# Performance work log

Measured on AMD Instinct MI355X. Metric: run time of the kernel, lower is better.

Reference implementation:

```python
import jax, jax.numpy as jnp
import numpy as np

C_M, C_Z, H, C = 256, 128, 8, 32  # msa emb, pair emb, heads, head channels
S, R = 128, 256                   # MSA rows, residues


def layer_norm(x, gamma, beta, eps=1e-5):
    mu = jnp.mean(x, axis=-1, keepdims=True)
    var = jnp.var(x, axis=-1, keepdims=True)
    return (x - mu) * jax.lax.rsqrt(var + eps) * gamma + beta


def setup_inputs() -> dict:
    key = jax.random.key(0)
    ks = jax.random.split(key, 12)
    sc_m = 1.0 / np.sqrt(C_M)
    sc_z = 1.0 / np.sqrt(C_Z)
    sc_hc = 1.0 / np.sqrt(H * C)
    return {
        "msa_rep": jax.random.normal(ks[0], (S, R, C_M), dtype=jnp.float32),
        "pair_rep": jax.random.normal(ks[1], (R, R, C_Z), dtype=jnp.float32),
        "ln_msa_g": jnp.ones((C_M,), jnp.float32),
        "ln_msa_b": jnp.zeros((C_M,), jnp.float32),
        "ln_pair_g": jnp.ones((C_Z,), jnp.float32),
        "ln_pair_b": jnp.zeros((C_Z,), jnp.float32),
        "w_q": jax.random.normal(ks[2], (C_M, H, C), jnp.float32) * sc_m,
        "w_k": jax.random.normal(ks[3], (C_M, H, C), jnp.float32) * sc_m,
        "w_v": jax.random.normal(ks[4], (C_M, H, C), jnp.float32) * sc_m,
        "w_g": jax.random.normal(ks[5], (C_M, H, C), jnp.float32) * sc_m,
        "b_g": jnp.zeros((H, C), jnp.float32),
        "w_b": jax.random.normal(ks[6], (C_Z, H), jnp.float32) * sc_z,
        "b_b": jnp.zeros((H,), jnp.float32),
        "w_o": jax.random.normal(ks[7], (H, C, C_M), jnp.float32) * sc_hc,
        "b_o": jnp.zeros((C_M,), jnp.float32),
    }


def reference(msa_rep, pair_rep, ln_msa_g, ln_msa_b, ln_pair_g, ln_pair_b,
              w_q, w_k, w_v, w_g, b_g, w_b, b_b, w_o, b_o):
    m = layer_norm(msa_rep, ln_msa_g, ln_msa_b)                 # [S,R,C_M]
    q = jnp.einsum('src,chd->srhd', m, w_q)                     # [S,R,H,C]
    k = jnp.einsum('src,chd->srhd', m, w_k)
    v = jnp.einsum('src,chd->srhd', m, w_v)
    gates = jax.nn.sigmoid(jnp.einsum('src,chd->srhd', m, w_g) + b_g)
    # pair bias: [R,R,H] -> [H,R,R]
    z = layer_norm(pair_rep, ln_pair_g, ln_pair_b)
    b = jnp.einsum('ijc,ch->hij', z, w_b) + b_b[:, None, None]  # [H,R,R]
    logits = jnp.einsum('sqhd,skhd->shqk', q, k) / np.sqrt(C)   # [S,H,R,R]
    logits = logits + b[None]
    w = jax.nn.softmax(logits, axis=-1)
    o = jnp.einsum('shqk,skhd->sqhd', w, v)                     # [S,R,H,C]
    o = gates * o
    out = jnp.einsum('srhd,hdc->src', o, w_o) + b_o             # [S,R,C_M]
    return out
```

## Files before the change

### kernel.cpp

```cpp
#include <hip/hip_runtime.h>
#include <hip/hip_bf16.h>

#define S_DIM 128
#define R_DIM 256
#define CM 256
#define CZ 128
#define H_DIM 8
#define C_DIM 32

typedef short bf16x8 __attribute__((ext_vector_type(8)));
typedef float f32x4 __attribute__((ext_vector_type(4)));

__device__ inline ushort f2b(float f) {
  __hip_bfloat16 b = __float2bfloat16(f);
  return *(ushort*)&b;
}
__device__ inline float b2f(ushort u) {
  __hip_bfloat16 b = *(__hip_bfloat16*)&u;
  return __bfloat162float(b);
}

__device__ __forceinline__ void gld_lds16(const ushort* g, ushort* l) {
  __builtin_amdgcn_global_load_lds(
      (const __attribute__((address_space(1))) unsigned int*)g,
      (__attribute__((address_space(3))) unsigned int*)l, 16, 0, 0);
}

__global__ __launch_bounds__(256) void wt_kernel(
    const float* __restrict__ wq, const float* __restrict__ wk,
    const float* __restrict__ wv, const float* __restrict__ wg,
    const float* __restrict__ wo, ushort* __restrict__ Wt5) {
  __shared__ float t[64][65];
  int z = blockIdx.z;
  const float* W = (z == 0) ? wq : (z == 1) ? wk : (z == 2) ? wv
                   : (z == 3) ? wg : wo;
  ushort* Wt = Wt5 + (size_t)z * 65536;
  int tid = threadIdx.x;
  int r = tid >> 2, c4 = (tid & 3) * 16;
  int rowBase = blockIdx.y * 64, colBase = blockIdx.x * 64;
#pragma unroll
  for (int j = 0; j < 16; ++j)
    t[r][c4 + j] = W[(size_t)(rowBase + r) * 256 + colBase + c4 + j];
  __syncthreads();
#pragma unroll
  for (int j = 0; j < 16; ++j)
    Wt[(size_t)(colBase + r) * 256 + rowBase + c4 + j] = f2b(t[c4 + j][r]);
}

__global__ __launch_bounds__(256) void ln_msa_kernel(
    const float* __restrict__ x, const float* __restrict__ g,
    const float* __restrict__ b, ushort* __restrict__ m) {
  int lane = threadIdx.x & 63, w = threadIdx.x >> 6;
  int row = blockIdx.x * 4 + w;
  const float* xp = x + (size_t)row * CM + lane * 4;
  float4 v = *(const float4*)xp;
  float s1 = v.x + v.y + v.z + v.w;
  float s2 = v.x * v.x + v.y * v.y + v.z * v.z + v.w * v.w;
#pragma unroll
  for (int off = 32; off; off >>= 1) {
    s1 += __shfl_xor(s1, off, 64);
    s2 += __shfl_xor(s2, off, 64);
  }
  float mean = s1 * (1.0f / CM);
  float rstd = rsqrtf(s2 * (1.0f / CM) - mean * mean + 1e-5f);
  float4 gv = *(const float4*)(g + lane * 4);
  float4 bv = *(const float4*)(b + lane * 4);
  ushort4 o;
  o.x = f2b((v.x - mean) * rstd * gv.x + bv.x);
  o.y = f2b((v.y - mean) * rstd * gv.y + bv.y);
  o.z = f2b((v.z - mean) * rstd * gv.z + bv.z);
  o.w = f2b((v.w - mean) * rstd * gv.w + bv.w);
  *(ushort4*)(m + (size_t)row * CM + lane * 4) = o;
}

__global__ __launch_bounds__(256) void pair_bias_kernel(
    const float* __restrict__ z, const float* __restrict__ g,
    const float* __restrict__ b, const float* __restrict__ w_b,
    const float* __restrict__ b_b, float* __restrict__ bias) {
  __shared__ float wbs[CZ][8];
  __shared__ float gs[CZ], bs[CZ];
  int tid = threadIdx.x;
  if (tid < CZ) { gs[tid] = g[tid]; bs[tid] = b[tid]; }
  for (int i = tid; i < CZ * 8; i += 256) wbs[i >> 3][i & 7] = w_b[i];
  __syncthreads();
  int q = tid & 3;
  int row = blockIdx.x * 64 + (tid >> 2);
  const float* zp = z + (size_t)row * CZ + q * 32;
  float4 v[8];
#pragma unroll
  for (int j = 0; j < 8; ++j) v[j] = *(const float4*)(zp + j * 4);
  float s1 = 0.f, s2 = 0.f;
#pragma unroll
  for (int j = 0; j < 8; ++j) {
    s1 += v[j].x + v[j].y + v[j].z + v[j].w;
    s2 += v[j].x * v[j].x + v[j].y * v[j].y + v[j].z * v[j].z +
          v[j].w * v[j].w;
  }
  s1 += __shfl_xor(s1, 1, 64);
  s2 += __shfl_xor(s2, 1, 64);
  s1 += __shfl_xor(s1, 2, 64);
  s2 += __shfl_xor(s2, 2, 64);
  float mean = s1 * (1.0f / CZ);
  float var = s2 * (1.0f / CZ) - mean * mean;
  float rstd = rsqrtf(var + 1e-5f);
  float acc[8] = {};
#pragma unroll
  for (int j = 0; j < 8; ++j) {
    float e[4] = {v[j].x, v[j].y, v[j].z, v[j].w};
#pragma unroll
    for (int u = 0; u < 4; ++u) {
      int c = q * 32 + j * 4 + u;
      float zn = (e[u] - mean) * rstd * gs[c] + bs[c];
#pragma unroll
      for (int h = 0; h < 8; ++h) acc[h] += zn * wbs[c][h];
    }
  }
#pragma unroll
  for (int h = 0; h < 8; ++h) {
    acc[h] += __shfl_xor(acc[h], 1, 64);
    acc[h] += __shfl_xor(acc[h], 2, 64);
  }
  int h0 = q * 2;
  bias[(size_t)h0 * (R_DIM * R_DIM) + row] = acc[h0] + b_b[h0];
  bias[(size_t)(h0 + 1) * (R_DIM * R_DIM) + row] = acc[h0 + 1] + b_b[h0 + 1];
}

__global__ __launch_bounds__(256) void proj_mfma(
    const ushort* __restrict__ M, const ushort* __restrict__ Wt5,
    const float* __restrict__ b_g, ushort* __restrict__ qb,
    ushort* __restrict__ kb2, ushort* __restrict__ vb,
    ushort* __restrict__ gb) {
  __shared__ ushort As[128 * 64];
  __shared__ ushort Bs[64 * 64];
  int tid = threadIdx.x, lane = tid & 63, wid = tid >> 6;
  int lr = lane & 15, lg = lane >> 4;
  int rowBase = blockIdx.x * 128;
  int cby = blockIdx.y;
  int proj = cby >> 2;
  int sc = (lane & 7) ^ ((lane >> 3) & 7);
  const ushort* Ag =
      M + (size_t)(rowBase + wid * 32 + (lane >> 3)) * 256 + sc * 8;
  const ushort* Bg =
      Wt5 + (size_t)(cby * 64 + wid * 16 + (lane >> 3)) * 256 + sc * 8;
  ushort* Asl = As + wid * (32 * 64);
  ushort* Bsl = Bs + wid * (16 * 64);
  int wr = wid >> 1, wc = wid & 1;
  int sx = (lr & 7) * 8;
  f32x4 zf = {0.f, 0.f, 0.f, 0.f};
  f32x4 acc[4][2];
#pragma unroll
  for (int i = 0; i < 4; ++i)
#pragma unroll
    for (int j = 0; j < 2; ++j) acc[i][j] = zf;

  for (int kb = 0; kb < 4; ++kb) {
    if (kb) __syncthreads();
#pragma unroll
    for (int c = 0; c < 4; ++c)
      gld_lds16(Ag + kb * 64 + c * (8 * 256), Asl + c * (8 * 64));
#pragma unroll
    for (int c = 0; c < 2; ++c)
      gld_lds16(Bg + kb * 64 + c * (8 * 256), Bsl + c * (8 * 64));
    __syncthreads();
#pragma unroll
    for (int kk = 0; kk < 2; ++kk) {
      bf16x8 a[4], b[2];
#pragma unroll
      for (int mf = 0; mf < 4; ++mf)
        a[mf] = *(const bf16x8*)&As[(wr * 64 + mf * 16 + lr) * 64 +
                                    ((kk * 32 + lg * 8) ^ sx)];
#pragma unroll
      for (int nf = 0; nf < 2; ++nf)
        b[nf] = *(const bf16x8*)&Bs[(wc * 32 + nf * 16 + lr) * 64 +
                                    ((kk * 32 + lg * 8) ^ sx)];
#pragma unroll
      for (int mf = 0; mf < 4; ++mf)
#pragma unroll
        for (int nf = 0; nf < 2; ++nf)
          acc[mf][nf] = __builtin_amdgcn_mfma_f32_16x16x32_bf16(
              b[nf], a[mf], acc[mf][nf], 0, 0, 0);
    }
  }
#pragma unroll
  for (int mf = 0; mf < 4; ++mf) {
    int row = rowBase + wr * 64 + mf * 16 + lr;
    int s = row >> 8, rr = row & 255;
#pragma unroll
    for (int nf = 0; nf < 2; ++nf) {
      int colL = (cby & 3) * 64 + wc * 32 + nf * 16 + lg * 4;
      int h = colL >> 5, d0 = colL & 31;
      size_t oidx = ((size_t)((s * H_DIM + h) * R_DIM + rr)) * C_DIM + d0;
      f32x4 v4 = acc[mf][nf];
      ushort4 o4;
      if (proj == 0) {
        o4.x = f2b(v4[0] * 0.17677669529663687f);
        o4.y = f2b(v4[1] * 0.17677669529663687f);
        o4.z = f2b(v4[2] * 0.17677669529663687f);
        o4.w = f2b(v4[3] * 0.17677669529663687f);
        *(ushort4*)(qb + oidx) = o4;
      } else if (proj == 1) {
        o4.x = f2b(v4[0]); o4.y = f2b(v4[1]);
        o4.z = f2b(v4[2]); o4.w = f2b(v4[3]);
        *(ushort4*)(kb2 + oidx) = o4;
      } else if (proj == 2) {
        o4.x = f2b(v4[0]); o4.y = f2b(v4[1]);
        o4.z = f2b(v4[2]); o4.w = f2b(v4[3]);
        *(ushort4*)(vb + oidx) = o4;
      } else {
        float4 bg4 = *(const float4*)(b_g + colL);
        o4.x = f2b(1.f / (1.f + __expf(-(v4[0] + bg4.x))));
        o4.y = f2b(1.f / (1.f + __expf(-(v4[1] + bg4.y))));
        o4.z = f2b(1.f / (1.f + __expf(-(v4[2] + bg4.z))));
        o4.w = f2b(1.f / (1.f + __expf(-(v4[3] + bg4.w))));
        *(ushort4*)(gb + oidx) = o4;
      }
    }
  }
}

__global__ __launch_bounds__(512, 4) void attn_mfma(
    const ushort* __restrict__ q, const ushort* __restrict__ k,
    const ushort* __restrict__ v, const ushort* __restrict__ g,
    const float* __restrict__ bias, ushort* __restrict__ ob) {
  __shared__ ushort Vt[32][264];
  __shared__ ushort Pl[8][32][72];
  int blk = blockIdx.x;
  int s = blk >> 3, h = blk & 7;
  int tid = threadIdx.x, lane = tid & 63, w = tid >> 6;
  int lr = lane & 15, lg = lane >> 4;
  size_t base = (size_t)(s * H_DIM + h) * (R_DIM * C_DIM);

  {
    int key = tid >> 1, half = (tid & 1) * 16;
    const ushort* vp = v + base + (size_t)key * 32 + half;
    bf16x8 t0 = *(const bf16x8*)vp;
    bf16x8 t1 = *(const bf16x8*)(vp + 8);
#pragma unroll
    for (int j = 0; j < 8; ++j) {
      Vt[half + j][key] = (ushort)t0[j];
      Vt[half + 8 + j][key] = (ushort)t1[j];
    }
  }
  __syncthreads();

  int qrow0 = w * 32;
  bf16x8 qf[2];
#pragma unroll
  for (int mf = 0; mf < 2; ++mf)
    qf[mf] = *(const bf16x8*)(q + base + (size_t)(qrow0 + mf * 16 + lr) * 32 +
                              lg * 8);
  const float* bp0 = bias + ((size_t)h * R_DIM + qrow0 + lg * 4) * R_DIM +
                     lr * 4;

  float lsum[2][4] = {};
  f32x4 of[2][2];
  f32x4 zf = {0.f, 0.f, 0.f, 0.f};
#pragma unroll
  for (int mf = 0; mf < 2; ++mf) {
    of[mf][0] = zf;
    of[mf][1] = zf;
  }

  bf16x8 kf[4];
#pragma unroll
  for (int nf = 0; nf < 4; ++nf)
    kf[nf] = *(const bf16x8*)(k + base + (size_t)(lr * 4 + nf) * 32 + lg * 8);

#pragma unroll
  for (int t = 0; t < 4; ++t) {
    int k0 = t * 64;
    bf16x8 kfn[4];
    if (t < 3) {
#pragma unroll
      for (int nf = 0; nf < 4; ++nf)
        kfn[nf] = *(const bf16x8*)(k + base +
                                   (size_t)(k0 + 64 + lr * 4 + nf) * 32 +
                                   lg * 8);
    }
    f32x4 sf[2][4];
    __builtin_amdgcn_s_setprio(1);
#pragma unroll
    for (int mf = 0; mf < 2; ++mf)
#pragma unroll
      for (int nf = 0; nf < 4; ++nf)
        sf[mf][nf] =
            __builtin_amdgcn_mfma_f32_16x16x32_bf16(qf[mf], kf[nf], zf, 0, 0, 0);
    __builtin_amdgcn_s_setprio(0);
#pragma unroll
    for (int mf = 0; mf < 2; ++mf) {
      float4 bv[4];
#pragma unroll
      for (int r = 0; r < 4; ++r)
        bv[r] = *(const float4*)(bp0 + (size_t)(mf * 16 + r) * R_DIM + k0);
#pragma unroll
      for (int r = 0; r < 4; ++r) {
        float p0 = __expf(sf[mf][0][r] + bv[r].x);
        float p1 = __expf(sf[mf][1][r] + bv[r].y);
        float p2 = __expf(sf[mf][2][r] + bv[r].z);
        float p3 = __expf(sf[mf][3][r] + bv[r].w);
        lsum[mf][r] += (p0 + p1) + (p2 + p3);
        ushort4 pk;
        pk.x = f2b(p0);
        pk.y = f2b(p1);
        pk.z = f2b(p2);
        pk.w = f2b(p3);
        *(ushort4*)&Pl[w][mf * 16 + lg * 4 + r][lr * 4] = pk;
      }
    }
    __builtin_amdgcn_s_setprio(1);
#pragma unroll
    for (int kt = 0; kt < 2; ++kt) {
      bf16x8 pf[2], vf[2];
#pragma unroll
      for (int mf = 0; mf < 2; ++mf)
        pf[mf] = *(const bf16x8*)&Pl[w][mf * 16 + lr][kt * 32 + lg * 8];
#pragma unroll
      for (int df = 0; df < 2; ++df)
        vf[df] = *(const bf16x8*)&Vt[df * 16 + lr][k0 + kt * 32 + lg * 8];
#pragma unroll
      for (int mf = 0; mf < 2; ++mf)
#pragma unroll
        for (int df = 0; df < 2; ++df)
          of[mf][df] = __builtin_amdgcn_mfma_f32_16x16x32_bf16(
              vf[df], pf[mf], of[mf][df], 0, 0, 0);
    }
    __builtin_amdgcn_s_setprio(0);
    if (t < 3) {
#pragma unroll
      for (int nf = 0; nf < 4; ++nf) kf[nf] = kfn[nf];
    }
  }
#pragma unroll
  for (int mf = 0; mf < 2; ++mf)
#pragma unroll
    for (int r = 0; r < 4; ++r) {
#pragma unroll
      for (int msk = 1; msk <= 8; msk <<= 1)
        lsum[mf][r] += __shfl_xor(lsum[mf][r], msk, 64);
    }
  int srcl = ((lr >> 2) << 4) + lr;
  float invr[2];
#pragma unroll
  for (int mf = 0; mf < 2; ++mf) {
    float t0 = __shfl(lsum[mf][0], srcl, 64);
    float t1 = __shfl(lsum[mf][1], srcl, 64);
    float t2 = __shfl(lsum[mf][2], srcl, 64);
    float t3 = __shfl(lsum[mf][3], srcl, 64);
    int rb = lr & 3;
    float lv = rb == 0 ? t0 : rb == 1 ? t1 : rb == 2 ? t2 : t3;
    invr[mf] = 1.f / lv;
  }
#pragma unroll
  for (int mf = 0; mf < 2; ++mf) {
    int row = qrow0 + mf * 16 + lr;
#pragma unroll
    for (int df = 0; df < 2; ++df) {
      int d0 = df * 16 + lg * 4;
      ushort4 g4 = *(const ushort4*)(g + base + (size_t)row * 32 + d0);
      ushort4 o4;
      o4.x = f2b(of[mf][df][0] * invr[mf] * b2f(g4.x));
      o4.y = f2b(of[mf][df][1] * invr[mf] * b2f(g4.y));
      o4.z = f2b(of[mf][df][2] * invr[mf] * b2f(g4.z));
      o4.w = f2b(of[mf][df][3] * invr[mf] * b2f(g4.w));
      *(ushort4*)(ob + ((size_t)(s * R_DIM + row)) * 256 + h * 32 + d0) = o4;
    }
  }
}

__global__ __launch_bounds__(256) void out_mfma(
    const ushort* __restrict__ A, const ushort* __restrict__ Wt,
    const float* __restrict__ b_o, float* __restrict__ out) {
  __shared__ ushort As[128 * 64];
  __shared__ ushort Bs[64 * 64];
  int tid = threadIdx.x, lane = tid & 63, wid = tid >> 6;
  int lr = lane & 15, lg = lane >> 4;
  int rowBase = blockIdx.x * 128;
  int colBase = blockIdx.y * 64;
  int sc = (lane & 7) ^ ((lane >> 3) & 7);
  const ushort* Ag =
      A + (size_t)(rowBase + wid * 32 + (lane >> 3)) * 256 + sc * 8;
  const ushort* Bg =
      Wt + (size_t)(colBase + wid * 16 + (lane >> 3)) * 256 + sc * 8;
  ushort* Asl = As + wid * (32 * 64);
  ushort* Bsl = Bs + wid * (16 * 64);
  int wr = wid >> 1, wc = wid & 1;
  int sx = (lr & 7) * 8;
  f32x4 zf = {0.f, 0.f, 0.f, 0.f};
  f32x4 acc[4][2];
#pragma unroll
  for (int i = 0; i < 4; ++i)
#pragma unroll
    for (int j = 0; j < 2; ++j) acc[i][j] = zf;

  for (int kb = 0; kb < 4; ++kb) {
    if (kb) __syncthreads();
#pragma unroll
    for (int c = 0; c < 4; ++c)
      gld_lds16(Ag + kb * 64 + c * (8 * 256), Asl + c * (8 * 64));
#pragma unroll
    for (int c = 0; c < 2; ++c)
      gld_lds16(Bg + kb * 64 + c * (8 * 256), Bsl + c * (8 * 64));
    __syncthreads();
#pragma unroll
    for (int kk = 0; kk < 2; ++kk) {
      bf16x8 a[4], b[2];
#pragma unroll
      for (int mf = 0; mf < 4; ++mf)
        a[mf] = *(const bf16x8*)&As[(wr * 64 + mf * 16 + lr) * 64 +
                                    ((kk * 32 + lg * 8) ^ sx)];
#pragma unroll
      for (int nf = 0; nf < 2; ++nf)
        b[nf] = *(const bf16x8*)&Bs[(wc * 32 + nf * 16 + lr) * 64 +
                                    ((kk * 32 + lg * 8) ^ sx)];
#pragma unroll
      for (int mf = 0; mf < 4; ++mf)
#pragma unroll
        for (int nf = 0; nf < 2; ++nf)
          acc[mf][nf] = __builtin_amdgcn_mfma_f32_16x16x32_bf16(
              b[nf], a[mf], acc[mf][nf], 0, 0, 0);
    }
  }
#pragma unroll
  for (int mf = 0; mf < 4; ++mf) {
    int row = rowBase + wr * 64 + mf * 16 + lr;
#pragma unroll
    for (int nf = 0; nf < 2; ++nf) {
      int col0 = colBase + wc * 32 + nf * 16 + lg * 4;
      float4 bo4 = *(const float4*)(b_o + col0);
      float4 o4;
      o4.x = acc[mf][nf][0] + bo4.x;
      o4.y = acc[mf][nf][1] + bo4.y;
      o4.z = acc[mf][nf][2] + bo4.z;
      o4.w = acc[mf][nf][3] + bo4.w;
      *(float4*)(out + (size_t)row * 256 + col0) = o4;
    }
  }
}

extern "C" void kernel_launch(void* const* d_in, const int* in_sizes, int n_in,
                              void* d_out, int out_size, void* d_ws,
                              size_t ws_size, hipStream_t stream) {
  const float* msa      = (const float*)d_in[0];
  const float* pair     = (const float*)d_in[1];
  const float* ln_msa_g = (const float*)d_in[2];
  const float* ln_msa_b = (const float*)d_in[3];
  const float* ln_pr_g  = (const float*)d_in[4];
  const float* ln_pr_b  = (const float*)d_in[5];
  const float* w_q      = (const float*)d_in[6];
  const float* w_k      = (const float*)d_in[7];
  const float* w_v      = (const float*)d_in[8];
  const float* w_g      = (const float*)d_in[9];
  const float* b_g      = (const float*)d_in[10];
  const float* w_b      = (const float*)d_in[11];
  const float* b_b      = (const float*)d_in[12];
  const float* w_o      = (const float*)d_in[13];
  const float* b_o      = (const float*)d_in[14];
  float* out = (float*)d_out;

  char* ws = (char*)d_ws;
  ushort* m   = (ushort*)(ws + 0);
  ushort* qb  = (ushort*)(ws + 16777216ull);
  ushort* kb  = (ushort*)(ws + 33554432ull);
  ushort* vb  = (ushort*)(ws + 50331648ull);
  ushort* gb  = (ushort*)(ws + 67108864ull);
  float*  bi  = (float*) (ws + 83886080ull);
  ushort* ob  = (ushort*)(ws + 85983232ull);
  ushort* Wt5 = (ushort*)(ws + 102760448ull);

  wt_kernel<<<dim3(4, 4, 5), 256, 0, stream>>>(w_q, w_k, w_v, w_g, w_o, Wt5);
  ln_msa_kernel<<<S_DIM * R_DIM / 4, 256, 0, stream>>>(msa, ln_msa_g,
                                                       ln_msa_b, m);
  pair_bias_kernel<<<R_DIM * R_DIM / 64, 256, 0, stream>>>(
      pair, ln_pr_g, ln_pr_b, w_b, b_b, bi);
  proj_mfma<<<dim3(256, 16), 256, 0, stream>>>(m, Wt5, b_g, qb, kb, vb, gb);
  attn_mfma<<<S_DIM * H_DIM, 512, 0, stream>>>(qb, kb, vb, gb, bi, ob);
  out_mfma<<<dim3(256, 4), 256, 0, stream>>>(ob, Wt5 + 4 * 65536, b_o, out);
}
```

Measured before the change: 117.5 us.

## Merge prologue kernels into one launch and switch softmax to exp2 domain

Folds the weight transpose, MSA layernorm and pair-bias kernels into a single prologue kernel that dispatches on block index. This removes two launches and the gaps between them. It also multiplies the pair bias and the query scale by log2(e), so the attention softmax can call exp2f instead of __expf and skip a multiply per element. The merged kernel allocates the largest shared-memory footprint for every block, which may reduce occupancy for the layernorm blocks.

```diff
diff --git a/kernel.cpp b/kernel.cpp
--- a/kernel.cpp
+++ b/kernel.cpp
@@ -20,109 +20,113 @@
   return __bfloat162float(b);
 }
 
+#define LOG2E 1.4426950408889634f
+
 __device__ __forceinline__ void gld_lds16(const ushort* g, ushort* l) {
   __builtin_amdgcn_global_load_lds(
       (const __attribute__((address_space(1))) unsigned int*)g,
       (__attribute__((address_space(3))) unsigned int*)l, 16, 0, 0);
 }
 
-__global__ __launch_bounds__(256) void wt_kernel(
+__global__ __launch_bounds__(256) void prologue_kernel(
+    const float* __restrict__ msa, const float* __restrict__ ln_msa_g,
+    const float* __restrict__ ln_msa_b, ushort* __restrict__ m,
+    const float* __restrict__ pair, const float* __restrict__ ln_pr_g,
+    const float* __restrict__ ln_pr_b, const float* __restrict__ w_b,
+    const float* __restrict__ b_b, float* __restrict__ bias,
     const float* __restrict__ wq, const float* __restrict__ wk,
     const float* __restrict__ wv, const float* __restrict__ wg,
     const float* __restrict__ wo, ushort* __restrict__ Wt5) {
   __shared__ float t[64][65];
-  int z = blockIdx.z;
-  const float* W = (z == 0) ? wq : (z == 1) ? wk : (z == 2) ? wv
-                   : (z == 3) ? wg : wo;
-  ushort* Wt = Wt5 + (size_t)z * 65536;
-  int tid = threadIdx.x;
-  int r = tid >> 2, c4 = (tid & 3) * 16;
-  int rowBase = blockIdx.y * 64, colBase = blockIdx.x * 64;
-#pragma unroll
-  for (int j = 0; j < 16; ++j)
-    t[r][c4 + j] = W[(size_t)(rowBase + r) * 256 + colBase + c4 + j];
-  __syncthreads();
-#pragma unroll
-  for (int j = 0; j < 16; ++j)
-    Wt[(size_t)(colBase + r) * 256 + rowBase + c4 + j] = f2b(t[c4 + j][r]);
-}
-
-__global__ __launch_bounds__(256) void ln_msa_kernel(
-    const float* __restrict__ x, const float* __restrict__ g,
-    const float* __restrict__ b, ushort* __restrict__ m) {
-  int lane = threadIdx.x & 63, w = threadIdx.x >> 6;
-  int row = blockIdx.x * 4 + w;
-  const float* xp = x + (size_t)row * CM + lane * 4;
-  float4 v = *(const float4*)xp;
-  float s1 = v.x + v.y + v.z + v.w;
-  float s2 = v.x * v.x + v.y * v.y + v.z * v.z + v.w * v.w;
-#pragma unroll
-  for (int off = 32; off; off >>= 1) {
-    s1 += __shfl_xor(s1, off, 64);
-    s2 += __shfl_xor(s2, off, 64);
-  }
-  float mean = s1 * (1.0f / CM);
-  float rstd = rsqrtf(s2 * (1.0f / CM) - mean * mean + 1e-5f);
-  float4 gv = *(const float4*)(g + lane * 4);
-  float4 bv = *(const float4*)(b + lane * 4);
-  ushort4 o;
-  o.x = f2b((v.x - mean) * rstd * gv.x + bv.x);
-  o.y = f2b((v.y - mean) * rstd * gv.y + bv.y);
-  o.z = f2b((v.z - mean) * rstd * gv.z + bv.z);
-  o.w = f2b((v.w - mean) * rstd * gv.w + bv.w);
-  *(ushort4*)(m + (size_t)row * CM + lane * 4) = o;
-}
-
-__global__ __launch_bounds__(256) void pair_bias_kernel(
-    const float* __restrict__ z, const float* __restrict__ g,
-    const float* __restrict__ b, const float* __restrict__ w_b,
-    const float* __restrict__ b_b, float* __restrict__ bias) {
   __shared__ float wbs[CZ][8];
   __shared__ float gs[CZ], bs[CZ];
+  int b = blockIdx.x;
   int tid = threadIdx.x;
-  if (tid < CZ) { gs[tid] = g[tid]; bs[tid] = b[tid]; }
-  for (int i = tid; i < CZ * 8; i += 256) wbs[i >> 3][i & 7] = w_b[i];
-  __syncthreads();
-  int q = tid & 3;
-  int row = blockIdx.x * 64 + (tid >> 2);
-  const float* zp = z + (size_t)row * CZ + q * 32;
-  float4 v[8];
-#pragma unroll
-  for (int j = 0; j < 8; ++j) v[j] = *(const float4*)(zp + j * 4);
-  float s1 = 0.f, s2 = 0.f;
-#pragma unroll
-  for (int j = 0; j < 8; ++j) {
-    s1 += v[j].x + v[j].y + v[j].z + v[j].w;
-    s2 += v[j].x * v[j].x + v[j].y * v[j].y + v[j].z * v[j].z +
-          v[j].w * v[j].w;
-  }
-  s1 += __shfl_xor(s1, 1, 64);
-  s2 += __shfl_xor(s2, 1, 64);
-  s1 += __shfl_xor(s1, 2, 64);
-  s2 += __shfl_xor(s2, 2, 64);
-  float mean = s1 * (1.0f / CZ);
-  float var = s2 * (1.0f / CZ) - mean * mean;
-  float rstd = rsqrtf(var + 1e-5f);
-  float acc[8] = {};
-#pragma unroll
-  for (int j = 0; j < 8; ++j) {
-    float e[4] = {v[j].x, v[j].y, v[j].z, v[j].w};
-#pragma unroll
-    for (int u = 0; u < 4; ++u) {
-      int c = q * 32 + j * 4 + u;
-      float zn = (e[u] - mean) * rstd * gs[c] + bs[c];
-#pragma unroll
-      for (int h = 0; h < 8; ++h) acc[h] += zn * wbs[c][h];
-    }
-  }
-#pragma unroll
-  for (int h = 0; h < 8; ++h) {
-    acc[h] += __shfl_xor(acc[h], 1, 64);
-    acc[h] += __shfl_xor(acc[h], 2, 64);
-  }
-  int h0 = q * 2;
-  bias[(size_t)h0 * (R_DIM * R_DIM) + row] = acc[h0] + b_b[h0];
-  bias[(size_t)(h0 + 1) * (R_DIM * R_DIM) + row] = acc[h0 + 1] + b_b[h0 + 1];
+  if (b < 8192) {
+    int lane = tid & 63, w = tid >> 6;
+    int row = b * 4 + w;
+    const float* xp = msa + (size_t)row * CM + lane * 4;
+    float4 v = *(const float4*)xp;
+    float s1 = v.x + v.y + v.z + v.w;
+    float s2 = v.x * v.x + v.y * v.y + v.z * v.z + v.w * v.w;
+#pragma unroll
+    for (int off = 32; off; off >>= 1) {
+      s1 += __shfl_xor(s1, off, 64);
+      s2 += __shfl_xor(s2, off, 64);
+    }
+    float mean = s1 * (1.0f / CM);
+    float rstd = rsqrtf(s2 * (1.0f / CM) - mean * mean + 1e-5f);
+    float4 gv = *(const float4*)(ln_msa_g + lane * 4);
+    float4 bv = *(const float4*)(ln_msa_b + lane * 4);
+    ushort4 o;
+    o.x = f2b((v.x - mean) * rstd * gv.x + bv.x);
+    o.y = f2b((v.y - mean) * rstd * gv.y + bv.y);
+    o.z = f2b((v.z - mean) * rstd * gv.z + bv.z);
+    o.w = f2b((v.w - mean) * rstd * gv.w + bv.w);
+    *(ushort4*)(m + (size_t)row * CM + lane * 4) = o;
+  } else if (b < 9216) {
+    int bb = b - 8192;
+    if (tid < CZ) { gs[tid] = ln_pr_g[tid]; bs[tid] = ln_pr_b[tid]; }
+    for (int i = tid; i < CZ * 8; i += 256) wbs[i >> 3][i & 7] = w_b[i];
+    __syncthreads();
+    int q = tid & 3;
+    int row = bb * 64 + (tid >> 2);
+    const float* zp = pair + (size_t)row * CZ + q * 32;
+    float4 v[8];
+#pragma unroll
+    for (int j = 0; j < 8; ++j) v[j] = *(const float4*)(zp + j * 4);
+    float s1 = 0.f, s2 = 0.f;
+#pragma unroll
+    for (int j = 0; j < 8; ++j) {
+      s1 += v[j].x + v[j].y + v[j].z + v[j].w;
+      s2 += v[j].x * v[j].x + v[j].y * v[j].y + v[j].z * v[j].z +
+            v[j].w * v[j].w;
+    }
+    s1 += __shfl_xor(s1, 1, 64);
+    s2 += __shfl_xor(s2, 1, 64);
+    s1 += __shfl_xor(s1, 2, 64);
+    s2 += __shfl_xor(s2, 2, 64);
+    float mean = s1 * (1.0f / CZ);
+    float var = s2 * (1.0f / CZ) - mean * mean;
+    float rstd = rsqrtf(var + 1e-5f);
+    float acc[8] = {};
+#pragma unroll
+    for (int j = 0; j < 8; ++j) {
+      float e[4] = {v[j].x, v[j].y, v[j].z, v[j].w};
+#pragma unroll
+      for (int u = 0; u < 4; ++u) {
+        int c = q * 32 + j * 4 + u;
+        float zn = (e[u] - mean) * rstd * gs[c] + bs[c];
+#pragma unroll
+        for (int h = 0; h < 8; ++h) acc[h] += zn * wbs[c][h];
+      }
+    }
+#pragma unroll
+    for (int h = 0; h < 8; ++h) {
+      acc[h] += __shfl_xor(acc[h], 1, 64);
+      acc[h] += __shfl_xor(acc[h], 2, 64);
+    }
+    int h0 = q * 2;
+    bias[(size_t)h0 * (R_DIM * R_DIM) + row] = (acc[h0] + b_b[h0]) * LOG2E;
+    bias[(size_t)(h0 + 1) * (R_DIM * R_DIM) + row] =
+        (acc[h0 + 1] + b_b[h0 + 1]) * LOG2E;
+  } else {
+    int zz = b - 9216;
+    int z = zz >> 4, rem = zz & 15;
+    int by = rem >> 2, bx = rem & 3;
+    const float* W = (z == 0) ? wq : (z == 1) ? wk : (z == 2) ? wv
+                     : (z == 3) ? wg : wo;
+    ushort* Wt = Wt5 + (size_t)z * 65536;
+    int r = tid >> 2, c4 = (tid & 3) * 16;
+    int rowBase = by * 64, colBase = bx * 64;
+#pragma unroll
+    for (int j = 0; j < 16; ++j)
+      t[r][c4 + j] = W[(size_t)(rowBase + r) * 256 + colBase + c4 + j];
+    __syncthreads();
+#pragma unroll
+    for (int j = 0; j < 16; ++j)
+      Wt[(size_t)(colBase + r) * 256 + rowBase + c4 + j] = f2b(t[c4 + j][r]);
+  }
 }
 
 __global__ __launch_bounds__(256) void proj_mfma(
@@ -193,10 +197,11 @@
       f32x4 v4 = acc[mf][nf];
       ushort4 o4;
       if (proj == 0) {
-        o4.x = f2b(v4[0] * 0.17677669529663687f);
-        o4.y = f2b(v4[1] * 0.17677669529663687f);
-        o4.z = f2b(v4[2] * 0.17677669529663687f);
-        o4.w = f2b(v4[3] * 0.17677669529663687f);
+        const float qs = 0.17677669529663687f * LOG2E;
+        o4.x = f2b(v4[0] * qs);
+        o4.y = f2b(v4[1] * qs);
+        o4.z = f2b(v4[2] * qs);
+        o4.w = f2b(v4[3] * qs);
         *(ushort4*)(qb + oidx) = o4;
       } else if (proj == 1) {
         o4.x = f2b(v4[0]); o4.y = f2b(v4[1]);
@@ -294,10 +299,10 @@
         bv[r] = *(const float4*)(bp0 + (size_t)(mf * 16 + r) * R_DIM + k0);
 #pragma unroll
       for (int r = 0; r < 4; ++r) {
-        float p0 = __expf(sf[mf][0][r] + bv[r].x);
-        float p1 = __expf(sf[mf][1][r] + bv[r].y);
-        float p2 = __expf(sf[mf][2][r] + bv[r].z);
-        float p3 = __expf(sf[mf][3][r] + bv[r].w);
+        float p0 = exp2f(sf[mf][0][r] + bv[r].x);
+        float p1 = exp2f(sf[mf][1][r] + bv[r].y);
+        float p2 = exp2f(sf[mf][2][r] + bv[r].z);
+        float p3 = exp2f(sf[mf][3][r] + bv[r].w);
         lsum[mf][r] += (p0 + p1) + (p2 + p3);
         ushort4 pk;
         pk.x = f2b(p0);
@@ -467,11 +472,9 @@
   ushort* ob  = (ushort*)(ws + 85983232ull);
   ushort* Wt5 = (ushort*)(ws + 102760448ull);
 
-  wt_kernel<<<dim3(4, 4, 5), 256, 0, stream>>>(w_q, w_k, w_v, w_g, w_o, Wt5);
-  ln_msa_kernel<<<S_DIM * R_DIM / 4, 256, 0, stream>>>(msa, ln_msa_g,
-                                                       ln_msa_b, m);
-  pair_bias_kernel<<<R_DIM * R_DIM / 64, 256, 0, stream>>>(
-      pair, ln_pr_g, ln_pr_b, w_b, b_b, bi);
+  prologue_kernel<<<9296, 256, 0, stream>>>(
+      msa, ln_msa_g, ln_msa_b, m, pair, ln_pr_g, ln_pr_b, w_b, b_b, bi,
+      w_q, w_k, w_v, w_g, w_o, Wt5);
   proj_mfma<<<dim3(256, 16), 256, 0, stream>>>(m, Wt5, b_g, qb, kb, vb, gb);
   attn_mfma<<<S_DIM * H_DIM, 512, 0, stream>>>(qb, kb, vb, gb, bi, ob);
   out_mfma<<<dim3(256, 4), 256, 0, stream>>>(ob, Wt5 + 4 * 65536, b_o, out);
```

New measurement: 118.0 us. No clear change (+0.4%).
